# Kernel tuning notes

Hardware: AMD Instinct MI355X
Metric: run time of the kernel (lower is better)

## Reference

```python
import jax, jax.numpy as jnp
import numpy as np

EPS = 1e-20


def squash(s):
    # n: [..., 1] norm over last axis
    n = jnp.linalg.norm(s, axis=-1, keepdims=True)
    return (1.0 - 1.0 / (jnp.exp(n) + EPS)) * (s / (n + EPS))


def setup_inputs() -> dict:
    key = jax.random.key(0)
    k1, k2 = jax.random.split(key)
    B, iN, iD, N, D = 1024, 128, 16, 32, 32
    inputs = jax.random.normal(k1, (B, iN, iD), dtype=jnp.float32)
    # he_normal: std = sqrt(2 / fan_in), fan_in = iN*iD (per keras conventions on 4D weight)
    fan_in = iN * iD
    W = jax.random.normal(k2, (N, iN, iD, D), dtype=jnp.float32) * np.sqrt(2.0 / fan_in).astype(np.float32)
    b = jnp.zeros((N, iN, 1), dtype=jnp.float32)
    return {"inputs": inputs, "W": W, "b": b}


def reference(inputs, W, b):
    D = W.shape[-1]
    # u[b,n,j,z] = sum_i inputs[b,j,i] * W[n,j,i,z]  -> [B, N, iN, D]
    u = jnp.einsum('bji,njiz->bnjz', inputs, W)
    # c[b,n,i] = sum_k sum_j u[b,n,i,j] * u[b,n,k,j] = u[b,n,i,:] . sum_k u[b,n,k,:]
    usum = jnp.sum(u, axis=2)                      # [B, N, D]
    c = jnp.einsum('bnid,bnd->bni', u, usum)[..., None]  # [B, N, iN, 1]
    c = c / jnp.sqrt(jnp.float32(D))
    c = jax.nn.softmax(c, axis=1)                  # softmax over parent-capsule axis N
    c = c + b                                      # b broadcasts over batch
    s = jnp.sum(u * c, axis=-2)                    # [B, N, D]
    return squash(s)
```

## Files before the change

kernel.cpp:

```cpp
#include <hip/hip_runtime.h>
#include <math.h>

#define B_TOT 1024
#define IN_N  128
#define IN_D  16
#define NCAP  32
#define DCAP  32

typedef __attribute__((ext_vector_type(8)))  short bf16x8;
typedef __attribute__((ext_vector_type(16))) float f32x16;
typedef unsigned int  uint_;
typedef unsigned short ushort_;

__device__ __forceinline__ uint_ cvt_pk_bf16(float lo, float hi) {
    uint_ r;
    asm("v_cvt_pk_bf16_f32 %0, %1, %2" : "=v"(r) : "v"(lo), "v"(hi));
    return r;
}
__device__ __forceinline__ float bf16_to_f(ushort_ h) {
    return __uint_as_float(((uint_)h) << 16);
}

__global__ __launch_bounds__(256)
void prep(const float* __restrict__ x, const float* __restrict__ W,
          ushort_* __restrict__ XW, ushort_* __restrict__ WT) {
    const int blk = blockIdx.x;
    const int t   = threadIdx.x;

    if (blk < 512) {
        const int q  = blk * 256 + t;
        const int z  = q & 31;
        const int nj = q >> 5;
        const float* p = W + (size_t)nj * (IN_D * DCAP) + z;
        float f[16];
#pragma unroll
        for (int i = 0; i < 16; ++i) f[i] = p[i * 32];
        uint4 lo, hi;
        lo.x = cvt_pk_bf16(f[0],  f[1]);  lo.y = cvt_pk_bf16(f[2],  f[3]);
        lo.z = cvt_pk_bf16(f[4],  f[5]);  lo.w = cvt_pk_bf16(f[6],  f[7]);
        hi.x = cvt_pk_bf16(f[8],  f[9]);  hi.y = cvt_pk_bf16(f[10], f[11]);
        hi.z = cvt_pk_bf16(f[12], f[13]); hi.w = cvt_pk_bf16(f[14], f[15]);
        uint4* dst = (uint4*)(WT + (size_t)q * 16);
        dst[0] = lo; dst[1] = hi;
        return;
    }

    const int id = blk - 512;
    const int tb = id >> 5;
    const int tc = id & 31;
    const int b0 = tb * 64, c0 = tc * 64;

    __shared__ ushort_ lds[64][72];

    {
        const int c4 = t & 15;
#pragma unroll
        for (int k = 0; k < 4; ++k) {
            const int r = (t >> 4) + 16 * k;
            const float4 f = *(const float4*)(x + (size_t)(b0 + r) * 2048 + c0 + c4 * 4);
            uint2 o;
            o.x = cvt_pk_bf16(f.x, f.y);
            o.y = cvt_pk_bf16(f.z, f.w);
            *(uint2*)&lds[r][c4 * 4] = o;
        }
    }
    __syncthreads();

    const int jb2l = t >> 5;
    const int jb20 = tc * 8;
#pragma unroll
    for (int h = 0; h < 2; ++h) {
        const int bl = (t & 31) + h * 32;
        bf16x8 v = *(const bf16x8*)&lds[bl][jb2l * 8];
        *(bf16x8*)(XW + ((size_t)(jb20 + jb2l) * 1024 + b0 + bl) * 8) = v;
    }
}

__global__ __launch_bounds__(256, 4)
void kA(const ushort_* __restrict__ XW, const ushort_* __restrict__ WT,
        ushort_* __restrict__ LC) {
    const int bid = blockIdx.x;
    const int n   = bid >> 5;
    const int cb0 = (bid & 31) * 32;
    const int t   = threadIdx.x;
    const int wv  = t >> 6;
    const int l   = t & 63;
    const int lo5 = l & 31;
    const int hi  = l >> 5;

    __shared__ float xch[4][16 * 64];

    const ushort_* aBase = WT + ((size_t)(n * IN_N) * 32 + lo5) * 16 + (size_t)hi * 8;
    const ushort_* bBase = XW + ((size_t)hi * 1024 + cb0 + lo5) * 8;

    const int jbeg = wv * 32;

    f32x16 us0, us1, us2, us3;
#pragma unroll
    for (int r = 0; r < 16; ++r) { us0[r] = 0.f; us1[r] = 0.f; us2[r] = 0.f; us3[r] = 0.f; }

    for (int j = jbeg; j < jbeg + 32; j += 4) {
        bf16x8 a0 = *(const bf16x8*)(aBase + (size_t)j * 512);
        bf16x8 x0 = *(const bf16x8*)(bBase + (size_t)j * 16384);
        bf16x8 a1 = *(const bf16x8*)(aBase + (size_t)(j + 1) * 512);
        bf16x8 x1 = *(const bf16x8*)(bBase + (size_t)(j + 1) * 16384);
        us0 = __builtin_amdgcn_mfma_f32_32x32x16_bf16(a0, x0, us0, 0, 0, 0);
        us1 = __builtin_amdgcn_mfma_f32_32x32x16_bf16(a1, x1, us1, 0, 0, 0);
        bf16x8 a2 = *(const bf16x8*)(aBase + (size_t)(j + 2) * 512);
        bf16x8 x2 = *(const bf16x8*)(bBase + (size_t)(j + 2) * 16384);
        bf16x8 a3 = *(const bf16x8*)(aBase + (size_t)(j + 3) * 512);
        bf16x8 x3 = *(const bf16x8*)(bBase + (size_t)(j + 3) * 16384);
        us2 = __builtin_amdgcn_mfma_f32_32x32x16_bf16(a2, x2, us2, 0, 0, 0);
        us3 = __builtin_amdgcn_mfma_f32_32x32x16_bf16(a3, x3, us3, 0, 0, 0);
    }
#pragma unroll
    for (int r = 0; r < 16; ++r)
        us0[r] = (us0[r] + us1[r]) + (us2[r] + us3[r]);

#pragma unroll
    for (int r = 0; r < 16; ++r) xch[wv][r * 64 + l] = us0[r];
    __syncthreads();

    f32x16 us;
#pragma unroll
    for (int r = 0; r < 16; ++r)
        us[r] = (xch[0][r * 64 + l] + xch[1][r * 64 + l]) +
                (xch[2][r * 64 + l] + xch[3][r * 64 + l]);

    const float rsqD = 0.17677669529663689f;
    f32x16 zc;
#pragma unroll
    for (int r = 0; r < 16; ++r) zc[r] = 0.f;

#pragma unroll 2
    for (int j = jbeg; j < jbeg + 32; ++j) {
        bf16x8 af = *(const bf16x8*)(aBase + (size_t)j * 512);
        bf16x8 xf = *(const bf16x8*)(bBase + (size_t)j * 16384);
        f32x16 u = __builtin_amdgcn_mfma_f32_32x32x16_bf16(af, xf, zc, 0, 0, 0);
        float p0 = u[0] * us[0], p1 = u[1] * us[1];
        float p2 = u[2] * us[2], p3 = u[3] * us[3];
#pragma unroll
        for (int r = 4; r < 16; r += 4) {
            p0 = fmaf(u[r],     us[r],     p0);
            p1 = fmaf(u[r + 1], us[r + 1], p1);
            p2 = fmaf(u[r + 2], us[r + 2], p2);
            p3 = fmaf(u[r + 3], us[r + 3], p3);
        }
        float p = (p0 + p1) + (p2 + p3);
        p += __shfl_xor(p, 32);
        p *= rsqD;
        if (l < 32) {
            uint_ pk = cvt_pk_bf16(p, p);
            LC[(size_t)(n * IN_N + j) * 1024 + cb0 + lo5] = (ushort_)(pk & 0xffffu);
        }
    }
}

__global__ __launch_bounds__(256)
void kB(const float* __restrict__ bias, ushort_* __restrict__ LC) {
    const int t  = blockIdx.x * 256 + threadIdx.x;
    const int j  = t >> 9;
    const int bp = (t & 511) * 2;
    float vl[NCAP], vh[NCAP];
    float ml = -1e30f, mh = -1e30f;
#pragma unroll
    for (int n = 0; n < NCAP; ++n) {
        const uint_ w = *(const uint_*)(LC + (size_t)(n * IN_N + j) * 1024 + bp);
        vl[n] = bf16_to_f((ushort_)(w & 0xffffu));
        vh[n] = bf16_to_f((ushort_)(w >> 16));
        ml = fmaxf(ml, vl[n]);
        mh = fmaxf(mh, vh[n]);
    }
    float sl = 0.f, sh = 0.f;
#pragma unroll
    for (int n = 0; n < NCAP; ++n) {
        vl[n] = __expf(vl[n] - ml); sl += vl[n];
        vh[n] = __expf(vh[n] - mh); sh += vh[n];
    }
    const float il = 1.f / sl, ih = 1.f / sh;
#pragma unroll
    for (int n = 0; n < NCAP; ++n) {
        const float bb = bias[n * IN_N + j];
        const float cl = vl[n] * il + bb;
        const float ch = vh[n] * ih + bb;
        *(uint_*)(LC + (size_t)(n * IN_N + j) * 1024 + bp) = cvt_pk_bf16(cl, ch);
    }
}

__global__ __launch_bounds__(256, 4)
void kC(const ushort_* __restrict__ XW, const ushort_* __restrict__ WT,
        const ushort_* __restrict__ LC, float* __restrict__ out) {
    const int bid = blockIdx.x;
    const int n   = bid >> 5;
    const int cb0 = (bid & 31) * 32;
    const int t   = threadIdx.x;
    const int wv  = t >> 6;
    const int l   = t & 63;
    const int lo5 = l & 31;
    const int hi  = l >> 5;

    __shared__ float xch[3][16 * 64];

    const ushort_* aBase = WT + ((size_t)(n * IN_N) * 32 + lo5) * 16 + (size_t)hi * 8;
    const ushort_* bBase = XW + ((size_t)hi * 1024 + cb0 + lo5) * 8;
    const ushort_* cBase = LC + (size_t)(n * IN_N) * 1024 + cb0 + lo5;

    f32x16 s0, s1, zc;
#pragma unroll
    for (int r = 0; r < 16; ++r) { s0[r] = 0.f; s1[r] = 0.f; zc[r] = 0.f; }

    const int jbeg = wv * 32;
    for (int j = jbeg; j < jbeg + 32; j += 2) {
        bf16x8 a0 = *(const bf16x8*)(aBase + (size_t)j * 512);
        bf16x8 x0 = *(const bf16x8*)(bBase + (size_t)j * 16384);
        const float c0 = bf16_to_f(cBase[(size_t)j * 1024]);
        bf16x8 a1 = *(const bf16x8*)(aBase + (size_t)(j + 1) * 512);
        bf16x8 x1 = *(const bf16x8*)(bBase + (size_t)(j + 1) * 16384);
        const float c1 = bf16_to_f(cBase[(size_t)(j + 1) * 1024]);
        f32x16 u0 = __builtin_amdgcn_mfma_f32_32x32x16_bf16(a0, x0, zc, 0, 0, 0);
        f32x16 u1 = __builtin_amdgcn_mfma_f32_32x32x16_bf16(a1, x1, zc, 0, 0, 0);
#pragma unroll
        for (int r = 0; r < 16; ++r) {
            s0[r] = fmaf(c0, u0[r], s0[r]);
            s1[r] = fmaf(c1, u1[r], s1[r]);
        }
    }
#pragma unroll
    for (int r = 0; r < 16; ++r) s0[r] += s1[r];

    if (wv > 0) {
#pragma unroll
        for (int r = 0; r < 16; ++r) xch[wv - 1][r * 64 + l] = s0[r];
    }
    __syncthreads();

    if (wv == 0) {
#pragma unroll
        for (int r = 0; r < 16; ++r)
            s0[r] += (xch[0][r * 64 + l] + xch[1][r * 64 + l]) + xch[2][r * 64 + l];
        float q0 = s0[0] * s0[0], q1 = s0[1] * s0[1];
        float q2 = s0[2] * s0[2], q3 = s0[3] * s0[3];
#pragma unroll
        for (int r = 4; r < 16; r += 4) {
            q0 = fmaf(s0[r],     s0[r],     q0);
            q1 = fmaf(s0[r + 1], s0[r + 1], q1);
            q2 = fmaf(s0[r + 2], s0[r + 2], q2);
            q3 = fmaf(s0[r + 3], s0[r + 3], q3);
        }
        float q = (q0 + q1) + (q2 + q3);
        q += __shfl_xor(q, 32);
        const float nn = sqrtf(q);
        const float f  = (1.f - 1.f / (__expf(nn) + 1e-20f)) / (nn + 1e-20f);
        float* op = out + ((size_t)(cb0 + lo5) * NCAP + n) * DCAP + hi * 4;
#pragma unroll
        for (int g = 0; g < 4; ++g) {
            float4 v4 = { s0[g * 4 + 0] * f, s0[g * 4 + 1] * f,
                          s0[g * 4 + 2] * f, s0[g * 4 + 3] * f };
            *(float4*)(op + g * 8) = v4;
        }
    }
}

extern "C" void kernel_launch(void* const* d_in, const int* in_sizes, int n_in,
                              void* d_out, int out_size, void* d_ws, size_t ws_size,
                              hipStream_t stream) {
    const float* x    = (const float*)d_in[0];
    const float* W    = (const float*)d_in[1];
    const float* bias = (const float*)d_in[2];
    float* out = (float*)d_out;

    char* ws = (char*)d_ws;
    ushort_* XW = (ushort_*)ws;
    ushort_* WT = (ushort_*)(ws + (4u << 20));
    ushort_* LC = (ushort_*)(ws + (8u << 20));

    prep<<<1024, 256, 0, stream>>>(x, W, XW, WT);
    kA<<<1024, 256, 0, stream>>>(XW, WT, LC);
    kB<<<256, 256, 0, stream>>>(bias, LC);
    kC<<<1024, 256, 0, stream>>>(XW, WT, LC, out);
}
```

Before: 59.28 us.

## Swizzle prep LDS, raise occupancy bounds, simplify kB and kC loops

Several independent changes land together. The prep transpose buffer becomes an XOR-swizzled uint2 array, meant to avoid LDS bank conflicts, and kA and kC raise their launch-bounds minimum blocks from 4 to 5, which may force register spills. kA's j loop now runs in reverse, and kC drops its dual-accumulator unroll in favour of one accumulator with unroll 2, shortening register pressure but also the independent FMA chains. kB handles one batch element per thread with twice the blocks, so its loads and stores become 2-byte instead of 4-byte.

```diff
diff --git a/kernel.cpp b/kernel.cpp
--- a/kernel.cpp
+++ b/kernel.cpp
@@ -50,7 +50,7 @@
     const int tc = id & 31;
     const int b0 = tb * 64, c0 = tc * 64;
 
-    __shared__ ushort_ lds[64][72];
+    __shared__ uint2 lds8[64][16];
 
     {
         const int c4 = t & 15;
@@ -61,7 +61,7 @@
             uint2 o;
             o.x = cvt_pk_bf16(f.x, f.y);
             o.y = cvt_pk_bf16(f.z, f.w);
-            *(uint2*)&lds[r][c4 * 4] = o;
+            lds8[r][c4 ^ (r & 15)] = o;
         }
     }
     __syncthreads();
@@ -71,12 +71,14 @@
 #pragma unroll
     for (int h = 0; h < 2; ++h) {
         const int bl = (t & 31) + h * 32;
-        bf16x8 v = *(const bf16x8*)&lds[bl][jb2l * 8];
-        *(bf16x8*)(XW + ((size_t)(jb20 + jb2l) * 1024 + b0 + bl) * 8) = v;
-    }
-}
-
-__global__ __launch_bounds__(256, 4)
+        const uint2 u0 = lds8[bl][(jb2l * 2)     ^ (bl & 15)];
+        const uint2 u1 = lds8[bl][(jb2l * 2 + 1) ^ (bl & 15)];
+        uint4 o; o.x = u0.x; o.y = u0.y; o.z = u1.x; o.w = u1.y;
+        *(uint4*)(XW + ((size_t)(jb20 + jb2l) * 1024 + b0 + bl) * 8) = o;
+    }
+}
+
+__global__ __launch_bounds__(256, 5)
 void kA(const ushort_* __restrict__ XW, const ushort_* __restrict__ WT,
         ushort_* __restrict__ LC) {
     const int bid = blockIdx.x;
@@ -133,7 +135,7 @@
     for (int r = 0; r < 16; ++r) zc[r] = 0.f;
 
 #pragma unroll 2
-    for (int j = jbeg; j < jbeg + 32; ++j) {
+    for (int j = jbeg + 31; j >= jbeg; --j) {
         bf16x8 af = *(const bf16x8*)(aBase + (size_t)j * 512);
         bf16x8 xf = *(const bf16x8*)(bBase + (size_t)j * 16384);
         f32x16 u = __builtin_amdgcn_mfma_f32_32x32x16_bf16(af, xf, zc, 0, 0, 0);
@@ -158,36 +160,29 @@
 
 __global__ __launch_bounds__(256)
 void kB(const float* __restrict__ bias, ushort_* __restrict__ LC) {
-    const int t  = blockIdx.x * 256 + threadIdx.x;
-    const int j  = t >> 9;
-    const int bp = (t & 511) * 2;
-    float vl[NCAP], vh[NCAP];
-    float ml = -1e30f, mh = -1e30f;
+    const int t = blockIdx.x * 256 + threadIdx.x;
+    const int j = t >> 10;
+    const int b = t & 1023;
+    float v[NCAP];
+    float m = -1e30f;
 #pragma unroll
     for (int n = 0; n < NCAP; ++n) {
-        const uint_ w = *(const uint_*)(LC + (size_t)(n * IN_N + j) * 1024 + bp);
-        vl[n] = bf16_to_f((ushort_)(w & 0xffffu));
-        vh[n] = bf16_to_f((ushort_)(w >> 16));
-        ml = fmaxf(ml, vl[n]);
-        mh = fmaxf(mh, vh[n]);
-    }
-    float sl = 0.f, sh = 0.f;
+        v[n] = bf16_to_f(LC[(size_t)(n * IN_N + j) * 1024 + b]);
+        m = fmaxf(m, v[n]);
+    }
+    float s = 0.f;
+#pragma unroll
+    for (int n = 0; n < NCAP; ++n) { v[n] = __expf(v[n] - m); s += v[n]; }
+    const float inv = 1.f / s;
 #pragma unroll
     for (int n = 0; n < NCAP; ++n) {
-        vl[n] = __expf(vl[n] - ml); sl += vl[n];
-        vh[n] = __expf(vh[n] - mh); sh += vh[n];
-    }
-    const float il = 1.f / sl, ih = 1.f / sh;
-#pragma unroll
-    for (int n = 0; n < NCAP; ++n) {
-        const float bb = bias[n * IN_N + j];
-        const float cl = vl[n] * il + bb;
-        const float ch = vh[n] * ih + bb;
-        *(uint_*)(LC + (size_t)(n * IN_N + j) * 1024 + bp) = cvt_pk_bf16(cl, ch);
-    }
-}
-
-__global__ __launch_bounds__(256, 4)
+        const float c = v[n] * inv + bias[n * IN_N + j];
+        uint_ pk = cvt_pk_bf16(c, c);
+        LC[(size_t)(n * IN_N + j) * 1024 + b] = (ushort_)(pk & 0xffffu);
+    }
+}
+
+__global__ __launch_bounds__(256, 5)
 void kC(const ushort_* __restrict__ XW, const ushort_* __restrict__ WT,
         const ushort_* __restrict__ LC, float* __restrict__ out) {
     const int bid = blockIdx.x;
@@ -205,28 +200,20 @@
     const ushort_* bBase = XW + ((size_t)hi * 1024 + cb0 + lo5) * 8;
     const ushort_* cBase = LC + (size_t)(n * IN_N) * 1024 + cb0 + lo5;
 
-    f32x16 s0, s1, zc;
-#pragma unroll
-    for (int r = 0; r < 16; ++r) { s0[r] = 0.f; s1[r] = 0.f; zc[r] = 0.f; }
+    f32x16 s0, zc;
+#pragma unroll
+    for (int r = 0; r < 16; ++r) { s0[r] = 0.f; zc[r] = 0.f; }
 
     const int jbeg = wv * 32;
-    for (int j = jbeg; j < jbeg + 32; j += 2) {
-        bf16x8 a0 = *(const bf16x8*)(aBase + (size_t)j * 512);
-        bf16x8 x0 = *(const bf16x8*)(bBase + (size_t)j * 16384);
-        const float c0 = bf16_to_f(cBase[(size_t)j * 1024]);
-        bf16x8 a1 = *(const bf16x8*)(aBase + (size_t)(j + 1) * 512);
-        bf16x8 x1 = *(const bf16x8*)(bBase + (size_t)(j + 1) * 16384);
-        const float c1 = bf16_to_f(cBase[(size_t)(j + 1) * 1024]);
-        f32x16 u0 = __builtin_amdgcn_mfma_f32_32x32x16_bf16(a0, x0, zc, 0, 0, 0);
-        f32x16 u1 = __builtin_amdgcn_mfma_f32_32x32x16_bf16(a1, x1, zc, 0, 0, 0);
-#pragma unroll
-        for (int r = 0; r < 16; ++r) {
-            s0[r] = fmaf(c0, u0[r], s0[r]);
-            s1[r] = fmaf(c1, u1[r], s1[r]);
-        }
-    }
-#pragma unroll
-    for (int r = 0; r < 16; ++r) s0[r] += s1[r];
+#pragma unroll 2
+    for (int j = jbeg; j < jbeg + 32; ++j) {
+        bf16x8 af = *(const bf16x8*)(aBase + (size_t)j * 512);
+        bf16x8 xf = *(const bf16x8*)(bBase + (size_t)j * 16384);
+        const float c = bf16_to_f(cBase[(size_t)j * 1024]);
+        f32x16 u = __builtin_amdgcn_mfma_f32_32x32x16_bf16(af, xf, zc, 0, 0, 0);
+#pragma unroll
+        for (int r = 0; r < 16; ++r) s0[r] = fmaf(c, u[r], s0[r]);
+    }
 
     if (wv > 0) {
 #pragma unroll
@@ -254,8 +241,7 @@
         float* op = out + ((size_t)(cb0 + lo5) * NCAP + n) * DCAP + hi * 4;
 #pragma unroll
         for (int g = 0; g < 4; ++g) {
-            float4 v4 = { s0[g * 4 + 0] * f, s0[g * 4 + 1] * f,
-                          s0[g * 4 + 2] * f, s0[g * 4 + 3] * f };
+            float4 v4 = { s0[g*4] * f, s0[g*4+1] * f, s0[g*4+2] * f, s0[g*4+3] * f };
             *(float4*)(op + g * 8) = v4;
         }
     }
@@ -276,6 +262,6 @@
 
     prep<<<1024, 256, 0, stream>>>(x, W, XW, WT);
     kA<<<1024, 256, 0, stream>>>(XW, WT, LC);
-    kB<<<256, 256, 0, stream>>>(bias, LC);
+    kB<<<512, 256, 0, stream>>>(bias, LC);
     kC<<<1024, 256, 0, stream>>>(XW, WT, LC, out);
 }
```

New measurement: 57.19 us. 3.5% less time.
